# Kernel optimization log

Hardware: AMD Instinct MI355X
Metric: run time of the kernel (lower is better)

Reference implementation:

```python
import jax, jax.numpy as jnp
import numpy as np

MEMORY_SIZE = 32768
FEATURE_DIM = 128
BATCH = 4096


def setup_inputs() -> dict:
    key = jax.random.key(0)
    k1, k2, k3, k4 = jax.random.split(key, 4)
    memory = jax.random.normal(k1, (MEMORY_SIZE, FEATURE_DIM), dtype=jnp.float32)
    input_data = jax.random.normal(k2, (BATCH, FEATURE_DIM), dtype=jnp.float32)
    write_weights = jax.random.uniform(k3, (BATCH, MEMORY_SIZE), dtype=jnp.float32)
    query = jax.random.normal(k4, (BATCH, FEATURE_DIM), dtype=jnp.float32)
    return {"memory": memory, "input_data": input_data,
            "write_weights": write_weights, "query": query}


def reference(memory, input_data, write_weights, query):
    # ---- write(): row-normalize weights, scatter-accumulate into memory ----
    # The original python double-loop computes update[j] += w[i,j] * x[i],
    # i.e. update = w_norm.T @ x  -- a single GEMM.
    w_norm = write_weights / jnp.sum(write_weights, axis=1, keepdims=True)
    update = jnp.einsum('bm,bf->mf', w_norm, input_data)  # [M, F]
    memory_new = memory + update

    # ---- read(): softmax attention over memory slots ----
    scores = jnp.matmul(query, memory_new.T)              # [B, M]
    attention_weights = jax.nn.softmax(scores, axis=1)
    retrieved_memory = jnp.matmul(attention_weights, memory_new)  # [B, F]
    confidence_scores = jnp.max(attention_weights, axis=1)        # [B]
    return retrieved_memory, confidence_scores, memory_new
```

## Files before the change

kernel.cpp:

```cpp
#include <hip/hip_runtime.h>
#include <hip/hip_bf16.h>
#include <math.h>

#define MEMSZ 32768
#define FDIM  128
#define BATCH 4096

typedef float f32x4 __attribute__((ext_vector_type(4)));
typedef _Float16 f16x8 __attribute__((ext_vector_type(8)));
typedef short bf16x8 __attribute__((ext_vector_type(8)));
typedef unsigned short u16t;
typedef unsigned int u32t;

static __device__ __forceinline__ u16t f2h_bits(float f) {
    union { _Float16 h; u16t u; } c;
    c.h = (_Float16)f;
    return c.u;
}

#define GLDS16(gsrc, ldst) \
  __builtin_amdgcn_global_load_lds((const __attribute__((address_space(1))) void*)(gsrc), \
                                   (__attribute__((address_space(3))) void*)(ldst), 16, 0, 0)

__global__ __launch_bounds__(256) void k_rowsum(const float* __restrict__ W,
                                                float* __restrict__ inv_s) {
    const int row = blockIdx.x;
    const float4* Wr = reinterpret_cast<const float4*>(W + (size_t)row * MEMSZ);
    float acc = 0.f;
    #pragma unroll 4
    for (int i = threadIdx.x; i < MEMSZ / 4; i += 256) {
        float4 v = Wr[i];
        acc += (v.x + v.y) + (v.z + v.w);
    }
    #pragma unroll
    for (int off = 32; off > 0; off >>= 1)
        acc += __shfl_down(acc, off, 64);
    __shared__ float wsum[4];
    const int lane = threadIdx.x & 63, wid = threadIdx.x >> 6;
    if (lane == 0) wsum[wid] = acc;
    __syncthreads();
    if (threadIdx.x == 0)
        inv_s[row] = 1.0f / (wsum[0] + wsum[1] + wsum[2] + wsum[3]);
}

__global__ __launch_bounds__(256) void k_prep(const float* __restrict__ X,
                                              const float* __restrict__ inv_s,
                                              unsigned char* __restrict__ XT64) {
    __shared__ float xs[64][132];
    const int T = blockIdx.x;
    const int b0 = T * 64;
    const int tid = threadIdx.x;
    #pragma unroll
    for (int i = 0; i < 8; ++i) {
        const int idx = tid + i * 256;
        const int row = idx >> 5, c4 = idx & 31;
        const float s = inv_s[b0 + row];
        float4 v = *reinterpret_cast<const float4*>(&X[(size_t)(b0 + row) * FDIM + c4 * 4]);
        v.x *= s; v.y *= s; v.z *= s; v.w *= s;
        *reinterpret_cast<float4*>(&xs[row][c4 * 4]) = v;
    }
    __syncthreads();
    #pragma unroll
    for (int i = 0; i < 4; ++i) {
        const int L = tid + i * 256;
        const int fh = L >> 9, ff = (L >> 7) & 3, ks = (L >> 6) & 1, ln = L & 63;
        const int f = fh * 64 + ff * 16 + (ln & 15);
        const int bi = ks * 32 + (ln >> 4) * 8;
        u32t pk[4];
        #pragma unroll
        for (int h = 0; h < 4; ++h) {
            const float lo = xs[bi + 2 * h][f];
            const float hi = xs[bi + 2 * h + 1][f];
            asm("v_cvt_pk_bf16_f32 %0, %1, %2" : "=v"(pk[h]) : "v"(lo), "v"(hi));
        }
        *reinterpret_cast<uint4*>(XT64 + (size_t)T * 16384 + (size_t)L * 16) =
            make_uint4(pk[0], pk[1], pk[2], pk[3]);
    }
}

#define K2B 64
#define K2M 64
__global__ __launch_bounds__(256, 4) void k_update_sk(
    const float* __restrict__ W, const unsigned char* __restrict__ XT64,
    float* __restrict__ P)
{
    __shared__ __align__(16) unsigned char wt[2][16384];

    const int tid = threadIdx.x;
    const int lane = tid & 63, w = tid >> 6;
    const int q16 = lane & 15, g = lane >> 4;
    const int wm = w >> 1, wf = w & 1;
    const int mblk = (blockIdx.x >> 1) * K2M;
    const int khalf = blockIdx.x & 1;
    const int base = khalf * 32;

    f32x4 acc[2][4];
    #pragma unroll
    for (int mf = 0; mf < 2; ++mf)
        #pragma unroll
        for (int ff = 0; ff < 4; ++ff) acc[mf][ff] = (f32x4){0.f, 0.f, 0.f, 0.f};

    const unsigned char* xbase = XT64 + (size_t)(wf * 8192 + lane * 16);

    auto stageW = [&](int buf, int t) {
        const int b0 = t * K2B;
        #pragma unroll
        for (int c = 0; c < 4; ++c) {
            const int gi = c * 256 + tid;
            const int b = gi >> 4;
            const int src = ((gi & 15) * 16) ^ ((b & 8) << 1);
            GLDS16((const unsigned char*)W + (size_t)(b0 + b) * (MEMSZ * 4) + (size_t)mblk * 4 + src,
                   &wt[buf][gi * 16]);
        }
    };
    auto loadB = [&](bf16x8 (&br)[4][2], int t) {
        const unsigned char* xp = xbase + (size_t)t * 16384;
        #pragma unroll
        for (int ff = 0; ff < 4; ++ff)
            #pragma unroll
            for (int ks = 0; ks < 2; ++ks)
                br[ff][ks] = *reinterpret_cast<const bf16x8*>(xp + ff * 2048 + ks * 1024);
    };
    auto compute = [&](int buf, bf16x8 (&br)[4][2]) {
        bf16x8 afr[2][2];
        const unsigned char* tb = &wt[buf][0];
        #pragma unroll
        for (int mf = 0; mf < 2; ++mf) {
            const int mm4 = (wm * 32 + mf * 16 + q16) * 4;
            #pragma unroll
            for (int ks = 0; ks < 2; ++ks) {
                float av[8];
                #pragma unroll
                for (int e = 0; e < 8; ++e) {
                    const int b = ks * 32 + g * 8 + e;
                    av[e] = *reinterpret_cast<const float*>(
                        tb + b * 256 + (mm4 ^ ((b & 8) << 1)));
                }
                union { u32t u[4]; bf16x8 v; } cv;
                #pragma unroll
                for (int h = 0; h < 4; ++h)
                    asm("v_cvt_pk_bf16_f32 %0, %1, %2" : "=v"(cv.u[h]) : "v"(av[2 * h]), "v"(av[2 * h + 1]));
                afr[mf][ks] = cv.v;
            }
        }
        #pragma unroll
        for (int mf = 0; mf < 2; ++mf)
            #pragma unroll
            for (int ff = 0; ff < 4; ++ff)
                #pragma unroll
                for (int ks = 0; ks < 2; ++ks)
                    acc[mf][ff] = __builtin_amdgcn_mfma_f32_16x16x32_bf16(
                        afr[mf][ks], br[ff][ks], acc[mf][ff], 0, 0, 0);
    };

    bf16x8 bA[4][2], bB_[4][2];
    stageW(0, base); loadB(bA, base);
    const int NT = 32;
    for (int t = 0; t < NT; t += 2) {
        __builtin_amdgcn_s_barrier();
        if (t + 1 < NT) {
            loadB(bB_, base + t + 1); stageW(1, base + t + 1);
            asm volatile("s_waitcnt vmcnt(12)" ::: "memory");
        } else asm volatile("s_waitcnt vmcnt(0)" ::: "memory");
        __builtin_amdgcn_s_barrier();
        __builtin_amdgcn_sched_barrier(0);
        compute(0, bA);
        __builtin_amdgcn_s_barrier();
        if (t + 2 < NT) {
            loadB(bA, base + t + 2); stageW(0, base + t + 2);
            asm volatile("s_waitcnt vmcnt(12)" ::: "memory");
        } else asm volatile("s_waitcnt vmcnt(0)" ::: "memory");
        __builtin_amdgcn_s_barrier();
        __builtin_amdgcn_sched_barrier(0);
        compute(1, bB_);
    }

    float* Pk = P + (size_t)khalf * MEMSZ * FDIM;
    #pragma unroll
    for (int mf = 0; mf < 2; ++mf) {
        #pragma unroll
        for (int ff = 0; ff < 4; ++ff) {
            const int m0 = mblk + wm * 32 + mf * 16 + g * 4;
            const int fcol = wf * 64 + ff * 16 + q16;
            #pragma unroll
            for (int r = 0; r < 4; ++r)
                Pk[(size_t)(m0 + r) * FDIM + fcol] = acc[mf][ff][r];
        }
    }
}

__global__ __launch_bounds__(256) void k_fin(const float* __restrict__ Mem,
                                             const float* __restrict__ P,
                                             float* __restrict__ MemNew,
                                             u16t* __restrict__ MemH,
                                             u16t* __restrict__ MemHT) {
    const int tid = threadIdx.x;
    const int lane = tid & 63, w = tid >> 6;
    const int q16 = lane & 15, g = lane >> 4;
    const int wm = w >> 1, wf = w & 1;
    const int mblk = blockIdx.x * 64;
    const float* P0 = P;
    const float* P1 = P + (size_t)MEMSZ * FDIM;
    #pragma unroll
    for (int mf = 0; mf < 2; ++mf) {
        #pragma unroll
        for (int ff = 0; ff < 4; ++ff) {
            const int m0 = mblk + wm * 32 + mf * 16 + g * 4;
            const int fcol = wf * 64 + ff * 16 + q16;
            ushort4 ht;
            u16t* htp = reinterpret_cast<u16t*>(&ht);
            #pragma unroll
            for (int r = 0; r < 4; ++r) {
                const size_t idx = (size_t)(m0 + r) * FDIM + fcol;
                const float v = Mem[idx] + P0[idx] + P1[idx];
                MemNew[idx] = v;
                const u16t hb = f2h_bits(v);
                MemH[idx] = hb;
                htp[r] = hb;
            }
            *reinterpret_cast<ushort4*>(&MemHT[(size_t)fcol * MEMSZ + m0]) = ht;
        }
    }
}

__global__ __launch_bounds__(256, 2) void k_update_mfma(
    const float* __restrict__ W, const unsigned char* __restrict__ XT64,
    const float* __restrict__ Mem, float* __restrict__ MemNew,
    u16t* __restrict__ MemH, u16t* __restrict__ MemHT)
{
    __shared__ __align__(16) unsigned char wt[2][16384];

    const int tid = threadIdx.x;
    const int lane = tid & 63, w = tid >> 6;
    const int q16 = lane & 15, g = lane >> 4;
    const int wm = w >> 1, wf = w & 1;
    const int mblk = blockIdx.x * K2M;

    f32x4 acc[2][4];
    #pragma unroll
    for (int mf = 0; mf < 2; ++mf)
        #pragma unroll
        for (int ff = 0; ff < 4; ++ff) acc[mf][ff] = (f32x4){0.f, 0.f, 0.f, 0.f};

    const unsigned char* xbase = XT64 + (size_t)(wf * 8192 + lane * 16);

    auto stageW = [&](int buf, int t) {
        const int b0 = t * K2B;
        #pragma unroll
        for (int c = 0; c < 4; ++c) {
            const int gi = c * 256 + tid;
            const int b = gi >> 4;
            const int src = ((gi & 15) * 16) ^ ((b & 8) << 1);
            GLDS16((const unsigned char*)W + (size_t)(b0 + b) * (MEMSZ * 4) + (size_t)mblk * 4 + src,
                   &wt[buf][gi * 16]);
        }
    };
    auto loadB = [&](bf16x8 (&br)[4][2], int t) {
        const unsigned char* xp = xbase + (size_t)t * 16384;
        #pragma unroll
        for (int ff = 0; ff < 4; ++ff)
            #pragma unroll
            for (int ks = 0; ks < 2; ++ks)
                br[ff][ks] = *reinterpret_cast<const bf16x8*>(xp + ff * 2048 + ks * 1024);
    };
    auto compute = [&](int buf, bf16x8 (&br)[4][2]) {
        bf16x8 afr[2][2];
        const unsigned char* tb = &wt[buf][0];
        #pragma unroll
        for (int mf = 0; mf < 2; ++mf) {
            const int mm4 = (wm * 32 + mf * 16 + q16) * 4;
            #pragma unroll
            for (int ks = 0; ks < 2; ++ks) {
                float av[8];
                #pragma unroll
                for (int e = 0; e < 8; ++e) {
                    const int b = ks * 32 + g * 8 + e;
                    av[e] = *reinterpret_cast<const float*>(
                        tb + b * 256 + (mm4 ^ ((b & 8) << 1)));
                }
                union { u32t u[4]; bf16x8 v; } cv;
                #pragma unroll
                for (int h = 0; h < 4; ++h)
                    asm("v_cvt_pk_bf16_f32 %0, %1, %2" : "=v"(cv.u[h]) : "v"(av[2 * h]), "v"(av[2 * h + 1]));
                afr[mf][ks] = cv.v;
            }
        }
        #pragma unroll
        for (int mf = 0; mf < 2; ++mf)
            #pragma unroll
            for (int ff = 0; ff < 4; ++ff)
                #pragma unroll
                for (int ks = 0; ks < 2; ++ks)
                    acc[mf][ff] = __builtin_amdgcn_mfma_f32_16x16x32_bf16(
                        afr[mf][ks], br[ff][ks], acc[mf][ff], 0, 0, 0);
    };

    bf16x8 bA[4][2], bB_[4][2];
    stageW(0, 0); loadB(bA, 0);
    const int NT = BATCH / K2B;
    for (int t = 0; t < NT; t += 2) {
        __builtin_amdgcn_s_barrier();
        if (t + 1 < NT) { loadB(bB_, t + 1); stageW(1, t + 1); }
        if (t + 1 < NT) asm volatile("s_waitcnt vmcnt(12)" ::: "memory");
        else            asm volatile("s_waitcnt vmcnt(0)"  ::: "memory");
        __builtin_amdgcn_s_barrier();
        __builtin_amdgcn_sched_barrier(0);
        compute(0, bA);
        __builtin_amdgcn_s_barrier();
        if (t + 2 < NT) { loadB(bA, t + 2); stageW(0, t + 2); }
        if (t + 2 < NT) asm volatile("s_waitcnt vmcnt(12)" ::: "memory");
        else            asm volatile("s_waitcnt vmcnt(0)"  ::: "memory");
        __builtin_amdgcn_s_barrier();
        __builtin_amdgcn_sched_barrier(0);
        compute(1, bB_);
    }

    #pragma unroll
    for (int mf = 0; mf < 2; ++mf) {
        #pragma unroll
        for (int ff = 0; ff < 4; ++ff) {
            const int m0 = mblk + wm * 32 + mf * 16 + g * 4;
            const int fcol = wf * 64 + ff * 16 + q16;
            ushort4 ht;
            u16t* htp = reinterpret_cast<u16t*>(&ht);
            #pragma unroll
            for (int r = 0; r < 4; ++r) {
                const size_t idx = (size_t)(m0 + r) * FDIM + fcol;
                const float v = acc[mf][ff][r] + Mem[idx];
                MemNew[idx] = v;
                const u16t hb = f2h_bits(v);
                MemH[idx] = hb;
                htp[r] = hb;
            }
            *reinterpret_cast<ushort4*>(&MemHT[(size_t)fcol * MEMSZ + m0]) = ht;
        }
    }
}

#define K2_IT 16
#define K2_MT 64
__global__ __launch_bounds__(256) void k_update_f32(const float* __restrict__ W,
                                                    const float* __restrict__ X,
                                                    const float* __restrict__ inv_s,
                                                    const float* __restrict__ Mem,
                                                    float* __restrict__ MemNew) {
    __shared__ float w_lds[2][K2_IT][K2_MT];
    __shared__ float x_lds[2][K2_IT][FDIM];
    const int j0 = blockIdx.x * K2_MT;
    const int tid = threadIdx.x;
    const int tf = tid & 15;
    const int tj = tid >> 4;

    float acc[4][8];
    #pragma unroll
    for (int a = 0; a < 4; ++a)
        #pragma unroll
        for (int b = 0; b < 8; ++b) acc[a][b] = 0.f;

    float4 pw, px0, px1;
    float ps0, ps1;
    const int wr = tid >> 4, wc4 = tid & 15;
    const int xr0 = tid >> 5, xc0 = tid & 31;
    const int xr1 = (tid + 256) >> 5, xc1 = tid & 31;

    auto load_tile = [&](int it) {
        const int i0 = it * K2_IT;
        pw  = *reinterpret_cast<const float4*>(&W[(size_t)(i0 + wr) * MEMSZ + j0 + wc4 * 4]);
        px0 = *reinterpret_cast<const float4*>(&X[(size_t)(i0 + xr0) * FDIM + xc0 * 4]);
        ps0 = inv_s[i0 + xr0];
        px1 = *reinterpret_cast<const float4*>(&X[(size_t)(i0 + xr1) * FDIM + xc1 * 4]);
        ps1 = inv_s[i0 + xr1];
    };
    auto write_tile = [&](int buf) {
        *reinterpret_cast<float4*>(&w_lds[buf][wr][wc4 * 4]) = pw;
        float4 v = px0; v.x *= ps0; v.y *= ps0; v.z *= ps0; v.w *= ps0;
        *reinterpret_cast<float4*>(&x_lds[buf][xr0][xc0 * 4]) = v;
        float4 u = px1; u.x *= ps1; u.y *= ps1; u.z *= ps1; u.w *= ps1;
        *reinterpret_cast<float4*>(&x_lds[buf][xr1][xc1 * 4]) = u;
    };

    load_tile(0);
    write_tile(0);
    __syncthreads();
    const int NT = BATCH / K2_IT;
    for (int it = 0; it < NT; ++it) {
        const int cur = it & 1;
        if (it + 1 < NT) load_tile(it + 1);
        #pragma unroll 4
        for (int i = 0; i < K2_IT; ++i) {
            const float4 wv = *reinterpret_cast<const float4*>(&w_lds[cur][i][tj * 4]);
            const float4 xa = *reinterpret_cast<const float4*>(&x_lds[cur][i][tf * 4]);
            const float4 xb = *reinterpret_cast<const float4*>(&x_lds[cur][i][tf * 4 + 64]);
            const float wj[4] = {wv.x, wv.y, wv.z, wv.w};
            #pragma unroll
            for (int a = 0; a < 4; ++a) {
                acc[a][0] += wj[a] * xa.x; acc[a][1] += wj[a] * xa.y;
                acc[a][2] += wj[a] * xa.z; acc[a][3] += wj[a] * xa.w;
                acc[a][4] += wj[a] * xb.x; acc[a][5] += wj[a] * xb.y;
                acc[a][6] += wj[a] * xb.z; acc[a][7] += wj[a] * xb.w;
            }
        }
        if (it + 1 < NT) write_tile(cur ^ 1);
        __syncthreads();
    }
    #pragma unroll
    for (int a = 0; a < 4; ++a) {
        const size_t j = (size_t)j0 + tj * 4 + a;
        const float4 m0 = *reinterpret_cast<const float4*>(&Mem[j * FDIM + tf * 4]);
        const float4 m1 = *reinterpret_cast<const float4*>(&Mem[j * FDIM + tf * 4 + 64]);
        float4 o0 = {acc[a][0] + m0.x, acc[a][1] + m0.y, acc[a][2] + m0.z, acc[a][3] + m0.w};
        float4 o1 = {acc[a][4] + m1.x, acc[a][5] + m1.y, acc[a][6] + m1.z, acc[a][7] + m1.w};
        *reinterpret_cast<float4*>(&MemNew[j * FDIM + tf * 4]) = o0;
        *reinterpret_cast<float4*>(&MemNew[j * FDIM + tf * 4 + 64]) = o1;
    }
}

__global__ __launch_bounds__(256) void k_attn_mfma(
    const float* __restrict__ Q, const u16t* __restrict__ Kh, const u16t* __restrict__ KhT,
    float* __restrict__ accP, float* __restrict__ mP, float* __restrict__ lP, int s_shift)
{
    __shared__ __align__(16) unsigned char kv_u8[2][16384];
    __shared__ __align__(16) unsigned char v_u8[2][16384];
    __shared__ __align__(16) unsigned char p_u8[4][2048];

    const int tid = threadIdx.x;
    const int w = tid >> 6, lane = tid & 63;
    const int q16 = lane & 15, g = lane >> 4;
    const int S = 1 << s_shift;
    const int s_idx = blockIdx.x & (S - 1);
    const int qb = blockIdx.x >> s_shift;
    const int chunk = MEMSZ >> s_shift;
    const int slot0 = s_idx * chunk;
    const int NT = chunk >> 6;

    f16x8 qfrag[2][4];
    #pragma unroll
    for (int qf = 0; qf < 2; ++qf) {
        const float* qrow = Q + (size_t)(qb * 128 + w * 32 + qf * 16 + q16) * FDIM;
        #pragma unroll
        for (int ks = 0; ks < 4; ++ks) {
            float tmp[8];
            *reinterpret_cast<float4*>(&tmp[0]) = *reinterpret_cast<const float4*>(&qrow[ks * 32 + g * 8]);
            *reinterpret_cast<float4*>(&tmp[4]) = *reinterpret_cast<const float4*>(&qrow[ks * 32 + g * 8 + 4]);
            f16x8 v;
            #pragma unroll
            for (int e = 0; e < 8; ++e) v[e] = (_Float16)tmp[e];
            qfrag[qf][ks] = v;
        }
    }

    auto stage = [&](int buf, int tile) {
        const unsigned char* kbase = (const unsigned char*)Kh + (size_t)(slot0 + tile * 64) * 256;
        const unsigned char* tbase = (const unsigned char*)KhT + (size_t)(slot0 + tile * 64) * 2;
        #pragma unroll
        for (int c = 0; c < 4; ++c) {
            const int C = w * 4 + c;
            const int pp = C * 1024 + lane * 16;
            {
                const int slot = pp >> 8;
                const int inner = (pp & 255) ^ ((slot & 7) << 4);
                GLDS16(kbase + slot * 256 + inner, &kv_u8[buf][C * 1024]);
            }
            {
                const int d = pp >> 7;
                const int inner = (pp & 127) ^ ((d & 7) << 4);
                GLDS16(tbase + (size_t)d * 65536 + inner, &v_u8[buf][C * 1024]);
            }
        }
    };

    float m_run[2] = {-3.0e38f, -3.0e38f};
    float l_run[2] = {0.f, 0.f};
    f32x4 acc_o[8][2];
    #pragma unroll
    for (int df = 0; df < 8; ++df)
        #pragma unroll
        for (int qf = 0; qf < 2; ++qf)
            acc_o[df][qf] = (f32x4){0.f, 0.f, 0.f, 0.f};

    stage(0, 0);
    asm volatile("s_waitcnt vmcnt(0)" ::: "memory");
    __builtin_amdgcn_s_barrier();
    __builtin_amdgcn_sched_barrier(0);

    int cur = 0;
    for (int t = 0; t < NT; ++t) {
        if (t + 1 < NT) stage(cur ^ 1, t + 1);

        f32x4 acc_s[4][2];
        #pragma unroll
        for (int sf = 0; sf < 4; ++sf) {
            acc_s[sf][0] = (f32x4){0.f, 0.f, 0.f, 0.f};
            acc_s[sf][1] = (f32x4){0.f, 0.f, 0.f, 0.f};
        }
        const unsigned char* kvb = &kv_u8[cur][0];
        #pragma unroll
        for (int ks = 0; ks < 4; ++ks) {
            #pragma unroll
            for (int sf = 0; sf < 4; ++sf) {
                const int slot = sf * 16 + q16;
                const f16x8 a = *reinterpret_cast<const f16x8*>(
                    kvb + slot * 256 + ((ks * 64 + g * 16) ^ ((slot & 7) << 4)));
                acc_s[sf][0] = __builtin_amdgcn_mfma_f32_16x16x32_f16(a, qfrag[0][ks], acc_s[sf][0], 0, 0, 0);
                acc_s[sf][1] = __builtin_amdgcn_mfma_f32_16x16x32_f16(a, qfrag[1][ks], acc_s[sf][1], 0, 0, 0);
            }
        }

        f16x8 pb[2][2];
        unsigned char* pw = &p_u8[w][0];
        #pragma unroll
        for (int qf = 0; qf < 2; ++qf) {
            float pmax = acc_s[0][qf][0];
            #pragma unroll
            for (int sf = 0; sf < 4; ++sf)
                #pragma unroll
                for (int r = 0; r < 4; ++r)
                    pmax = fmaxf(pmax, acc_s[sf][qf][r]);
            pmax = fmaxf(pmax, __shfl_xor(pmax, 16));
            pmax = fmaxf(pmax, __shfl_xor(pmax, 32));
            const float mn = fmaxf(m_run[qf], pmax);
            float p[4][4];
            float psum = 0.f;
            #pragma unroll
            for (int sf = 0; sf < 4; ++sf)
                #pragma unroll
                for (int r = 0; r < 4; ++r) {
                    p[sf][r] = __expf(acc_s[sf][qf][r] - mn);
                    psum += p[sf][r];
                }
            psum += __shfl_xor(psum, 16);
            psum += __shfl_xor(psum, 32);
            const float sc = __expf(m_run[qf] - mn);
            l_run[qf] = l_run[qf] * sc + psum;
            m_run[qf] = mn;
            #pragma unroll
            for (int df = 0; df < 8; ++df) {
                acc_o[df][qf][0] *= sc; acc_o[df][qf][1] *= sc;
                acc_o[df][qf][2] *= sc; acc_o[df][qf][3] *= sc;
            }
            #pragma unroll
            for (int sf = 0; sf < 4; ++sf)
                #pragma unroll
                for (int rr = 0; rr < 2; ++rr) {
                    const u32t val = (u32t)f2h_bits(p[sf][2 * rr]) | ((u32t)f2h_bits(p[sf][2 * rr + 1]) << 16);
                    const int byte = q16 * 128 + (((sf * 16 + g * 4 + 2 * rr) * 2) ^ ((q16 & 7) << 4));
                    *reinterpret_cast<u32t*>(pw + byte) = val;
                }
            #pragma unroll
            for (int kk = 0; kk < 2; ++kk) {
                const int byte = q16 * 128 + (((kk * 32 + g * 8) * 2) ^ ((q16 & 7) << 4));
                pb[qf][kk] = *reinterpret_cast<const f16x8*>(pw + byte);
            }
        }

        const unsigned char* vb = &v_u8[cur][0];
        #pragma unroll
        for (int df = 0; df < 8; ++df) {
            #pragma unroll
            for (int kk = 0; kk < 2; ++kk) {
                const int d = df * 16 + q16;
                const f16x8 av = *reinterpret_cast<const f16x8*>(
                    vb + d * 128 + ((kk * 64 + g * 16) ^ ((d & 7) << 4)));
                acc_o[df][0] = __builtin_amdgcn_mfma_f32_16x16x32_f16(av, pb[0][kk], acc_o[df][0], 0, 0, 0);
                acc_o[df][1] = __builtin_amdgcn_mfma_f32_16x16x32_f16(av, pb[1][kk], acc_o[df][1], 0, 0, 0);
            }
        }

        asm volatile("s_waitcnt vmcnt(0)" ::: "memory");
        __builtin_amdgcn_s_barrier();
        __builtin_amdgcn_sched_barrier(0);
        cur ^= 1;
    }

    const int rowbase = qb * 128 + w * 32;
    #pragma unroll
    for (int qf = 0; qf < 2; ++qf) {
        const int row = rowbase + qf * 16 + q16;
        float* ap = accP + ((size_t)s_idx * BATCH + row) * FDIM;
        #pragma unroll
        for (int df = 0; df < 8; ++df) {
            float4 o = {acc_o[df][qf][0], acc_o[df][qf][1], acc_o[df][qf][2], acc_o[df][qf][3]};
            *reinterpret_cast<float4*>(&ap[df * 16 + g * 4]) = o;
        }
        if (g == 0) {
            mP[(size_t)s_idx * BATCH + row] = m_run[qf];
            lP[(size_t)s_idx * BATCH + row] = l_run[qf];
        }
    }
}

__global__ __launch_bounds__(256) void k_combine(const float* __restrict__ mP,
                                                 const float* __restrict__ lP,
                                                 const float* __restrict__ accP,
                                                 float* __restrict__ Out,
                                                 float* __restrict__ Conf, int S) {
    const int row = blockIdx.x * 8 + (threadIdx.x >> 5);
    const int lane = threadIdx.x & 31;
    float mt = -3.0e38f;
    for (int s = 0; s < S; ++s) mt = fmaxf(mt, mP[(size_t)s * BATCH + row]);
    float lt = 0.f;
    for (int s = 0; s < S; ++s) lt += lP[(size_t)s * BATCH + row] * __expf(mP[(size_t)s * BATCH + row] - mt);
    const float inv = 1.0f / lt;
    float4 o = {0.f, 0.f, 0.f, 0.f};
    for (int s = 0; s < S; ++s) {
        const float wgt = __expf(mP[(size_t)s * BATCH + row] - mt);
        const float4 a = *reinterpret_cast<const float4*>(&accP[((size_t)s * BATCH + row) * FDIM + lane * 4]);
        o.x += wgt * a.x; o.y += wgt * a.y; o.z += wgt * a.z; o.w += wgt * a.w;
    }
    float4 res = {o.x * inv, o.y * inv, o.z * inv, o.w * inv};
    *reinterpret_cast<float4*>(&Out[(size_t)row * FDIM + lane * 4]) = res;
    if (lane == 0) Conf[row] = inv;
}

#define QT 16
#define MT 64
#define LSTR (FDIM + 4)
__global__ __launch_bounds__(256) void k_attn_f32(const float* __restrict__ Q,
                                                  const float* __restrict__ MemNew,
                                                  float* __restrict__ Out,
                                                  float* __restrict__ Conf) {
    __shared__ float mem_lds[MT][LSTR];
    __shared__ float q_lds[QT][LSTR];
    __shared__ float p_lds[QT][MT];
    __shared__ float m_lds[QT], l_lds[QT], scale_lds[QT];

    const int tid = threadIdx.x;
    const int qblk = blockIdx.x * QT;

    #pragma unroll
    for (int r = 0; r < 2; ++r) {
        const int idx = tid + r * 256;
        const int row = idx >> 5, c4 = idx & 31;
        *reinterpret_cast<float4*>(&q_lds[row][c4 * 4]) =
            *reinterpret_cast<const float4*>(&Q[(size_t)(qblk + row) * FDIM + c4 * 4]);
    }
    if (tid < QT) { m_lds[tid] = -3.0e38f; l_lds[tid] = 0.f; }

    const int sq = (tid >> 5) * 2;
    const int sm = tid & 31;
    const int pq = tid >> 4;
    const int pf = (tid & 15) * 4;

    float acc[8];
    #pragma unroll
    for (int e = 0; e < 8; ++e) acc[e] = 0.f;

    for (int mt = 0; mt < MEMSZ / MT; ++mt) {
        __syncthreads();
        const float* src = MemNew + (size_t)mt * MT * FDIM;
        #pragma unroll
        for (int r = 0; r < 8; ++r) {
            const int idx = tid + r * 256;
            const int row = idx >> 5, c4 = idx & 31;
            *reinterpret_cast<float4*>(&mem_lds[row][c4 * 4]) =
                *reinterpret_cast<const float4*>(&src[(size_t)row * FDIM + c4 * 4]);
        }
        const float mold0 = m_lds[sq], mold1 = m_lds[sq + 1];
        __syncthreads();

        float s00 = 0.f, s01 = 0.f, s10 = 0.f, s11 = 0.f;
        #pragma unroll 8
        for (int k = 0; k < FDIM; k += 4) {
            const float4 qa = *reinterpret_cast<const float4*>(&q_lds[sq][k]);
            const float4 qb = *reinterpret_cast<const float4*>(&q_lds[sq + 1][k]);
            const float4 ma = *reinterpret_cast<const float4*>(&mem_lds[sm][k]);
            const float4 mb = *reinterpret_cast<const float4*>(&mem_lds[sm + 32][k]);
            s00 += qa.x*ma.x + qa.y*ma.y + qa.z*ma.z + qa.w*ma.w;
            s01 += qa.x*mb.x + qa.y*mb.y + qa.z*mb.z + qa.w*mb.w;
            s10 += qb.x*ma.x + qb.y*ma.y + qb.z*ma.z + qb.w*ma.w;
            s11 += qb.x*mb.x + qb.y*mb.y + qb.z*mb.z + qb.w*mb.w;
        }
        float r0 = fmaxf(s00, s01), r1 = fmaxf(s10, s11);
        #pragma unroll
        for (int off = 1; off <= 16; off <<= 1) {
            r0 = fmaxf(r0, __shfl_xor(r0, off, 64));
            r1 = fmaxf(r1, __shfl_xor(r1, off, 64));
        }
        const float mn0 = fmaxf(mold0, r0), mn1 = fmaxf(mold1, r1);
        const float p00 = __expf(s00 - mn0), p01 = __expf(s01 - mn0);
        const float p10 = __expf(s10 - mn1), p11 = __expf(s11 - mn1);
        float t0 = p00 + p01, t1 = p10 + p11;
        #pragma unroll
        for (int off = 1; off <= 16; off <<= 1) {
            t0 += __shfl_xor(t0, off, 64);
            t1 += __shfl_xor(t1, off, 64);
        }
        p_lds[sq][sm]      = p00; p_lds[sq][sm + 32]     = p01;
        p_lds[sq + 1][sm]  = p10; p_lds[sq + 1][sm + 32] = p11;
        if (sm == 0) {
            const float sc0 = __expf(mold0 - mn0), sc1 = __expf(mold1 - mn1);
            m_lds[sq] = mn0; m_lds[sq + 1] = mn1;
            l_lds[sq]     = l_lds[sq]     * sc0 + t0;
            l_lds[sq + 1] = l_lds[sq + 1] * sc1 + t1;
            scale_lds[sq] = sc0; scale_lds[sq + 1] = sc1;
        }
        __syncthreads();

        const float sc = scale_lds[pq];
        #pragma unroll
        for (int e = 0; e < 8; ++e) acc[e] *= sc;
        #pragma unroll 8
        for (int m = 0; m < MT; ++m) {
            const float p = p_lds[pq][m];
            const float4 va = *reinterpret_cast<const float4*>(&mem_lds[m][pf]);
            const float4 vb = *reinterpret_cast<const float4*>(&mem_lds[m][pf + 64]);
            acc[0] += p * va.x; acc[1] += p * va.y; acc[2] += p * va.z; acc[3] += p * va.w;
            acc[4] += p * vb.x; acc[5] += p * vb.y; acc[6] += p * vb.z; acc[7] += p * vb.w;
        }
    }
    const float linv = 1.0f / l_lds[pq];
    float4 o0 = {acc[0]*linv, acc[1]*linv, acc[2]*linv, acc[3]*linv};
    float4 o1 = {acc[4]*linv, acc[5]*linv, acc[6]*linv, acc[7]*linv};
    *reinterpret_cast<float4*>(&Out[(size_t)(qblk + pq) * FDIM + pf]) = o0;
    *reinterpret_cast<float4*>(&Out[(size_t)(qblk + pq) * FDIM + pf + 64]) = o1;
    if (tid < QT) Conf[qblk + tid] = 1.0f / l_lds[tid];
}

extern "C" void kernel_launch(void* const* d_in, const int* in_sizes, int n_in,
                              void* d_out, int out_size, void* d_ws, size_t ws_size,
                              hipStream_t stream) {
    (void)in_sizes; (void)n_in; (void)out_size;
    const float* memory   = (const float*)d_in[0];
    const float* input    = (const float*)d_in[1];
    const float* wweights = (const float*)d_in[2];
    const float* query    = (const float*)d_in[3];

    float* out       = (float*)d_out;
    float* retrieved = out;
    float* conf      = out + (size_t)BATCH * FDIM;
    float* mem_new   = conf + BATCH;

    char* ws = (char*)d_ws;
    float* inv_s = (float*)ws;
    const size_t off_xt   = 16384;
    const size_t off_h    = off_xt + (size_t)FDIM * BATCH * 2;
    const size_t off_hT   = off_h + (size_t)MEMSZ * FDIM * 2;
    const size_t off_part = off_hT + (size_t)MEMSZ * FDIM * 2;
    const size_t sz_p16   = (size_t)16 * ((size_t)BATCH * 8 + (size_t)BATCH * FDIM * 4);
    const size_t off_pk   = off_part + sz_p16;
    const size_t need_full = off_pk + (size_t)2 * MEMSZ * FDIM * 4;

    k_rowsum<<<BATCH, 256, 0, stream>>>(wweights, inv_s);

    if (ws_size >= need_full) {
        unsigned char* xt64 = (unsigned char*)(ws + off_xt);
        u16t* mh  = (u16t*)(ws + off_h);
        u16t* mhT = (u16t*)(ws + off_hT);
        float* mP   = (float*)(ws + off_part);
        float* lP   = mP + (size_t)16 * BATCH;
        float* accP = lP + (size_t)16 * BATCH;
        float* pk   = (float*)(ws + off_pk);
        k_prep<<<BATCH / 64, 256, 0, stream>>>(input, inv_s, xt64);
        k_update_sk<<<(MEMSZ / K2M) * 2, 256, 0, stream>>>(wweights, xt64, pk);
        k_fin<<<MEMSZ / 64, 256, 0, stream>>>(memory, pk, mem_new, mh, mhT);
        k_attn_mfma<<<(BATCH / 128) * 16, 256, 0, stream>>>(query, mh, mhT, accP, mP, lP, 4);
        k_combine<<<BATCH / 8, 256, 0, stream>>>(mP, lP, accP, retrieved, conf, 16);
        return;
    }

    int s_shift = -1;
    for (int sh = 4; sh >= 0; --sh) {
        const size_t S = (size_t)1 << sh;
        const size_t need = off_part + S * ((size_t)BATCH * 8 + (size_t)BATCH * FDIM * 4);
        if (ws_size >= need) { s_shift = sh; break; }
    }
    if (s_shift >= 0) {
        const int S = 1 << s_shift;
        unsigned char* xt64 = (unsigned char*)(ws + off_xt);
        u16t* mh  = (u16t*)(ws + off_h);
        u16t* mhT = (u16t*)(ws + off_hT);
        float* mP   = (float*)(ws + off_part);
        float* lP   = mP + (size_t)S * BATCH;
        float* accP = lP + (size_t)S * BATCH;
        k_prep<<<BATCH / 64, 256, 0, stream>>>(input, inv_s, xt64);
        k_update_mfma<<<MEMSZ / K2M, 256, 0, stream>>>(wweights, xt64, memory, mem_new, mh, mhT);
        k_attn_mfma<<<(BATCH / 128) * S, 256, 0, stream>>>(query, mh, mhT, accP, mP, lP, s_shift);
        k_combine<<<BATCH / 8, 256, 0, stream>>>(mP, lP, accP, retrieved, conf, S);
    } else {
        k_update_f32<<<MEMSZ / K2_MT, 256, 0, stream>>>(wweights, input, inv_s, memory, mem_new);
        k_attn_f32<<<BATCH / QT, 256, 0, stream>>>(query, mem_new, retrieved, conf);
    }
}
```

Measured before the change: 455.0 us.

## Fuse rowsum with bf16 transpose of write weights; drop split-K update

The row-sum kernel now also writes a transposed bf16 copy of the write weights, emitting per-tile partial sums that a small kernel reduces into inverse row sums. The update GEMM then streams this half-size, pre-transposed bf16 matrix over the full batch without split-K. That removes the fp32 partial buffers and the separate finalize kernel, since memory is added in the epilogue. The attention kernel also raises wave priority around its MFMA loops. The cost is an extra 256 MB bf16 write and read of the weights, and fewer blocks in the update kernel, which lowers its parallelism.

```diff
diff --git a/kernel.cpp b/kernel.cpp
--- a/kernel.cpp
+++ b/kernel.cpp
@@ -22,25 +22,72 @@
   __builtin_amdgcn_global_load_lds((const __attribute__((address_space(1))) void*)(gsrc), \
                                    (__attribute__((address_space(3))) void*)(ldst), 16, 0, 0)
 
-__global__ __launch_bounds__(256) void k_rowsum(const float* __restrict__ W,
-                                                float* __restrict__ inv_s) {
-    const int row = blockIdx.x;
-    const float4* Wr = reinterpret_cast<const float4*>(W + (size_t)row * MEMSZ);
-    float acc = 0.f;
-    #pragma unroll 4
-    for (int i = threadIdx.x; i < MEMSZ / 4; i += 256) {
-        float4 v = Wr[i];
-        acc += (v.x + v.y) + (v.z + v.w);
-    }
-    #pragma unroll
-    for (int off = 32; off > 0; off >>= 1)
-        acc += __shfl_down(acc, off, 64);
-    __shared__ float wsum[4];
-    const int lane = threadIdx.x & 63, wid = threadIdx.x >> 6;
-    if (lane == 0) wsum[wid] = acc;
+__global__ __launch_bounds__(256, 2) void k_rowsumT(const float* __restrict__ W,
+                                                    float* __restrict__ partial,
+                                                    u16t* __restrict__ WT) {
+    __shared__ __align__(16) unsigned char xs[65536];
+    __shared__ float red[128];
+    const int tid = threadIdx.x;
+    const int bt = blockIdx.x & 31, mt = blockIdx.x >> 5;
+    const int b0 = bt * 128, m0 = mt * 128;
+
+    #pragma unroll
+    for (int c = 0; c < 16; ++c) {
+        const int gi = c * 256 + tid;
+        const int b = gi >> 5;
+        const int inner = ((gi & 31) * 16) ^ ((b & 7) << 4);
+        GLDS16((const unsigned char*)W + ((size_t)(b0 + b) * MEMSZ + m0) * 4 + inner,
+               &xs[gi * 16]);
+    }
+    asm volatile("s_waitcnt vmcnt(0)" ::: "memory");
     __syncthreads();
-    if (threadIdx.x == 0)
-        inv_s[row] = 1.0f / (wsum[0] + wsum[1] + wsum[2] + wsum[3]);
+
+    {
+        const int b = tid >> 1, half = tid & 1;
+        float s = 0.f;
+        #pragma unroll
+        for (int i = 0; i < 16; ++i) {
+            const int off = b * 512 + ((half * 256 + i * 16) ^ ((b & 7) << 4));
+            const float4 v = *reinterpret_cast<const float4*>(&xs[off]);
+            s += (v.x + v.y) + (v.z + v.w);
+        }
+        s += __shfl_xor(s, 1, 64);
+        if (half == 0) red[b] = s;
+    }
+
+    {
+        const int m = tid & 127, bh = tid >> 7;
+        u16t* dstrow = WT + (size_t)(m0 + m) * BATCH + b0 + bh * 64;
+        #pragma unroll
+        for (int ch = 0; ch < 8; ++ch) {
+            u32t pk[4];
+            #pragma unroll
+            for (int h = 0; h < 4; ++h) {
+                const int b1 = bh * 64 + ch * 8 + 2 * h;
+                const float lo = *reinterpret_cast<const float*>(
+                    &xs[(size_t)b1 * 512 + ((m * 4) ^ ((b1 & 7) << 4))]);
+                const float hi = *reinterpret_cast<const float*>(
+                    &xs[(size_t)(b1 + 1) * 512 + ((m * 4) ^ (((b1 + 1) & 7) << 4))]);
+                asm("v_cvt_pk_bf16_f32 %0, %1, %2" : "=v"(pk[h]) : "v"(lo), "v"(hi));
+            }
+            *reinterpret_cast<uint4*>(dstrow + ch * 8) = make_uint4(pk[0], pk[1], pk[2], pk[3]);
+        }
+    }
+    __syncthreads();
+    if (tid < 128) partial[(size_t)mt * BATCH + b0 + tid] = red[tid];
+}
+
+__global__ __launch_bounds__(256) void k_inv(const float* __restrict__ partial,
+                                             float* __restrict__ inv_s) {
+    const int b = blockIdx.x * 256 + threadIdx.x;
+    float s0 = 0.f, s1 = 0.f, s2 = 0.f, s3 = 0.f;
+    for (int mt = 0; mt < 256; mt += 4) {
+        s0 += partial[(size_t)mt * BATCH + b];
+        s1 += partial[(size_t)(mt + 1) * BATCH + b];
+        s2 += partial[(size_t)(mt + 2) * BATCH + b];
+        s3 += partial[(size_t)(mt + 3) * BATCH + b];
+    }
+    inv_s[b] = 1.0f / ((s0 + s1) + (s2 + s3));
 }
 
 __global__ __launch_bounds__(256) void k_prep(const float* __restrict__ X,
@@ -80,19 +127,18 @@
 
 #define K2B 64
 #define K2M 64
-__global__ __launch_bounds__(256, 4) void k_update_sk(
-    const float* __restrict__ W, const unsigned char* __restrict__ XT64,
-    float* __restrict__ P)
+__global__ __launch_bounds__(256, 2) void k_update_wt(
+    const u16t* __restrict__ WT, const unsigned char* __restrict__ XT64,
+    const float* __restrict__ Mem, float* __restrict__ MemNew,
+    u16t* __restrict__ MemH, u16t* __restrict__ MemHT)
 {
-    __shared__ __align__(16) unsigned char wt[2][16384];
+    __shared__ __align__(16) unsigned char wt[2][8192];
 
     const int tid = threadIdx.x;
     const int lane = tid & 63, w = tid >> 6;
     const int q16 = lane & 15, g = lane >> 4;
     const int wm = w >> 1, wf = w & 1;
-    const int mblk = (blockIdx.x >> 1) * K2M;
-    const int khalf = blockIdx.x & 1;
-    const int base = khalf * 32;
+    const int mblk = blockIdx.x * K2M;
 
     f32x4 acc[2][4];
     #pragma unroll
@@ -103,13 +149,13 @@
     const unsigned char* xbase = XT64 + (size_t)(wf * 8192 + lane * 16);
 
     auto stageW = [&](int buf, int t) {
-        const int b0 = t * K2B;
-        #pragma unroll
-        for (int c = 0; c < 4; ++c) {
+        #pragma unroll
+        for (int c = 0; c < 2; ++c) {
             const int gi = c * 256 + tid;
-            const int b = gi >> 4;
-            const int src = ((gi & 15) * 16) ^ ((b & 8) << 1);
-            GLDS16((const unsigned char*)W + (size_t)(b0 + b) * (MEMSZ * 4) + (size_t)mblk * 4 + src,
+            const int m_loc = gi >> 3;
+            const int inner = ((gi & 7) * 16) ^ ((m_loc & 7) << 4);
+            GLDS16((const unsigned char*)WT + (size_t)(mblk + m_loc) * (BATCH * 2)
+                       + (size_t)t * 128 + inner,
                    &wt[buf][gi * 16]);
         }
     };
@@ -126,21 +172,11 @@
         const unsigned char* tb = &wt[buf][0];
         #pragma unroll
         for (int mf = 0; mf < 2; ++mf) {
-            const int mm4 = (wm * 32 + mf * 16 + q16) * 4;
+            const int m_loc = wm * 32 + mf * 16 + q16;
             #pragma unroll
             for (int ks = 0; ks < 2; ++ks) {
-                float av[8];
-                #pragma unroll
-                for (int e = 0; e < 8; ++e) {
-                    const int b = ks * 32 + g * 8 + e;
-                    av[e] = *reinterpret_cast<const float*>(
-                        tb + b * 256 + (mm4 ^ ((b & 8) << 1)));
-                }
-                union { u32t u[4]; bf16x8 v; } cv;
-                #pragma unroll
-                for (int h = 0; h < 4; ++h)
-                    asm("v_cvt_pk_bf16_f32 %0, %1, %2" : "=v"(cv.u[h]) : "v"(av[2 * h]), "v"(av[2 * h + 1]));
-                afr[mf][ks] = cv.v;
+                const int byte = m_loc * 128 + ((ks * 64 + g * 16) ^ ((m_loc & 7) << 4));
+                afr[mf][ks] = *reinterpret_cast<const bf16x8*>(tb + byte);
             }
         }
         #pragma unroll
@@ -154,53 +190,25 @@
     };
 
     bf16x8 bA[4][2], bB_[4][2];
-    stageW(0, base); loadB(bA, base);
-    const int NT = 32;
+    stageW(0, 0); loadB(bA, 0);
+    const int NT = BATCH / K2B;
     for (int t = 0; t < NT; t += 2) {
         __builtin_amdgcn_s_barrier();
-        if (t + 1 < NT) {
-            loadB(bB_, base + t + 1); stageW(1, base + t + 1);
-            asm volatile("s_waitcnt vmcnt(12)" ::: "memory");
-        } else asm volatile("s_waitcnt vmcnt(0)" ::: "memory");
+        if (t + 1 < NT) { loadB(bB_, t + 1); stageW(1, t + 1); }
+        if (t + 1 < NT) asm volatile("s_waitcnt vmcnt(10)" ::: "memory");
+        else            asm volatile("s_waitcnt vmcnt(0)"  ::: "memory");
         __builtin_amdgcn_s_barrier();
         __builtin_amdgcn_sched_barrier(0);
         compute(0, bA);
         __builtin_amdgcn_s_barrier();
-        if (t + 2 < NT) {
-            loadB(bA, base + t + 2); stageW(0, base + t + 2);
-            asm volatile("s_waitcnt vmcnt(12)" ::: "memory");
-        } else asm volatile("s_waitcnt vmcnt(0)" ::: "memory");
+        if (t + 2 < NT) { loadB(bA, t + 2); stageW(0, t + 2); }
+        if (t + 2 < NT) asm volatile("s_waitcnt vmcnt(10)" ::: "memory");
+        else            asm volatile("s_waitcnt vmcnt(0)"  ::: "memory");
         __builtin_amdgcn_s_barrier();
         __builtin_amdgcn_sched_barrier(0);
         compute(1, bB_);
     }
 
-    float* Pk = P + (size_t)khalf * MEMSZ * FDIM;
-    #pragma unroll
-    for (int mf = 0; mf < 2; ++mf) {
-        #pragma unroll
-        for (int ff = 0; ff < 4; ++ff) {
-            const int m0 = mblk + wm * 32 + mf * 16 + g * 4;
-            const int fcol = wf * 64 + ff * 16 + q16;
-            #pragma unroll
-            for (int r = 0; r < 4; ++r)
-                Pk[(size_t)(m0 + r) * FDIM + fcol] = acc[mf][ff][r];
-        }
-    }
-}
-
-__global__ __launch_bounds__(256) void k_fin(const float* __restrict__ Mem,
-                                             const float* __restrict__ P,
-                                             float* __restrict__ MemNew,
-                                             u16t* __restrict__ MemH,
-                                             u16t* __restrict__ MemHT) {
-    const int tid = threadIdx.x;
-    const int lane = tid & 63, w = tid >> 6;
-    const int q16 = lane & 15, g = lane >> 4;
-    const int wm = w >> 1, wf = w & 1;
-    const int mblk = blockIdx.x * 64;
-    const float* P0 = P;
-    const float* P1 = P + (size_t)MEMSZ * FDIM;
     #pragma unroll
     for (int mf = 0; mf < 2; ++mf) {
         #pragma unroll
@@ -212,7 +220,7 @@
             #pragma unroll
             for (int r = 0; r < 4; ++r) {
                 const size_t idx = (size_t)(m0 + r) * FDIM + fcol;
-                const float v = Mem[idx] + P0[idx] + P1[idx];
+                const float v = acc[mf][ff][r] + Mem[idx];
                 MemNew[idx] = v;
                 const u16t hb = f2h_bits(v);
                 MemH[idx] = hb;
@@ -337,84 +345,6 @@
     }
 }
 
-#define K2_IT 16
-#define K2_MT 64
-__global__ __launch_bounds__(256) void k_update_f32(const float* __restrict__ W,
-                                                    const float* __restrict__ X,
-                                                    const float* __restrict__ inv_s,
-                                                    const float* __restrict__ Mem,
-                                                    float* __restrict__ MemNew) {
-    __shared__ float w_lds[2][K2_IT][K2_MT];
-    __shared__ float x_lds[2][K2_IT][FDIM];
-    const int j0 = blockIdx.x * K2_MT;
-    const int tid = threadIdx.x;
-    const int tf = tid & 15;
-    const int tj = tid >> 4;
-
-    float acc[4][8];
-    #pragma unroll
-    for (int a = 0; a < 4; ++a)
-        #pragma unroll
-        for (int b = 0; b < 8; ++b) acc[a][b] = 0.f;
-
-    float4 pw, px0, px1;
-    float ps0, ps1;
-    const int wr = tid >> 4, wc4 = tid & 15;
-    const int xr0 = tid >> 5, xc0 = tid & 31;
-    const int xr1 = (tid + 256) >> 5, xc1 = tid & 31;
-
-    auto load_tile = [&](int it) {
-        const int i0 = it * K2_IT;
-        pw  = *reinterpret_cast<const float4*>(&W[(size_t)(i0 + wr) * MEMSZ + j0 + wc4 * 4]);
-        px0 = *reinterpret_cast<const float4*>(&X[(size_t)(i0 + xr0) * FDIM + xc0 * 4]);
-        ps0 = inv_s[i0 + xr0];
-        px1 = *reinterpret_cast<const float4*>(&X[(size_t)(i0 + xr1) * FDIM + xc1 * 4]);
-        ps1 = inv_s[i0 + xr1];
-    };
-    auto write_tile = [&](int buf) {
-        *reinterpret_cast<float4*>(&w_lds[buf][wr][wc4 * 4]) = pw;
-        float4 v = px0; v.x *= ps0; v.y *= ps0; v.z *= ps0; v.w *= ps0;
-        *reinterpret_cast<float4*>(&x_lds[buf][xr0][xc0 * 4]) = v;
-        float4 u = px1; u.x *= ps1; u.y *= ps1; u.z *= ps1; u.w *= ps1;
-        *reinterpret_cast<float4*>(&x_lds[buf][xr1][xc1 * 4]) = u;
-    };
-
-    load_tile(0);
-    write_tile(0);
-    __syncthreads();
-    const int NT = BATCH / K2_IT;
-    for (int it = 0; it < NT; ++it) {
-        const int cur = it & 1;
-        if (it + 1 < NT) load_tile(it + 1);
-        #pragma unroll 4
-        for (int i = 0; i < K2_IT; ++i) {
-            const float4 wv = *reinterpret_cast<const float4*>(&w_lds[cur][i][tj * 4]);
-            const float4 xa = *reinterpret_cast<const float4*>(&x_lds[cur][i][tf * 4]);
-            const float4 xb = *reinterpret_cast<const float4*>(&x_lds[cur][i][tf * 4 + 64]);
-            const float wj[4] = {wv.x, wv.y, wv.z, wv.w};
-            #pragma unroll
-            for (int a = 0; a < 4; ++a) {
-                acc[a][0] += wj[a] * xa.x; acc[a][1] += wj[a] * xa.y;
-                acc[a][2] += wj[a] * xa.z; acc[a][3] += wj[a] * xa.w;
-                acc[a][4] += wj[a] * xb.x; acc[a][5] += wj[a] * xb.y;
-                acc[a][6] += wj[a] * xb.z; acc[a][7] += wj[a] * xb.w;
-            }
-        }
-        if (it + 1 < NT) write_tile(cur ^ 1);
-        __syncthreads();
-    }
-    #pragma unroll
-    for (int a = 0; a < 4; ++a) {
-        const size_t j = (size_t)j0 + tj * 4 + a;
-        const float4 m0 = *reinterpret_cast<const float4*>(&Mem[j * FDIM + tf * 4]);
-        const float4 m1 = *reinterpret_cast<const float4*>(&Mem[j * FDIM + tf * 4 + 64]);
-        float4 o0 = {acc[a][0] + m0.x, acc[a][1] + m0.y, acc[a][2] + m0.z, acc[a][3] + m0.w};
-        float4 o1 = {acc[a][4] + m1.x, acc[a][5] + m1.y, acc[a][6] + m1.z, acc[a][7] + m1.w};
-        *reinterpret_cast<float4*>(&MemNew[j * FDIM + tf * 4]) = o0;
-        *reinterpret_cast<float4*>(&MemNew[j * FDIM + tf * 4 + 64]) = o1;
-    }
-}
-
 __global__ __launch_bounds__(256) void k_attn_mfma(
     const float* __restrict__ Q, const u16t* __restrict__ Kh, const u16t* __restrict__ KhT,
     float* __restrict__ accP, float* __restrict__ mP, float* __restrict__ lP, int s_shift)
@@ -494,6 +424,7 @@
             acc_s[sf][1] = (f32x4){0.f, 0.f, 0.f, 0.f};
         }
         const unsigned char* kvb = &kv_u8[cur][0];
+        __builtin_amdgcn_s_setprio(1);
         #pragma unroll
         for (int ks = 0; ks < 4; ++ks) {
             #pragma unroll
@@ -505,6 +436,7 @@
                 acc_s[sf][1] = __builtin_amdgcn_mfma_f32_16x16x32_f16(a, qfrag[1][ks], acc_s[sf][1], 0, 0, 0);
             }
         }
+        __builtin_amdgcn_s_setprio(0);
 
         f16x8 pb[2][2];
         unsigned char* pw = &p_u8[w][0];
@@ -554,6 +486,7 @@
         }
 
         const unsigned char* vb = &v_u8[cur][0];
+        __builtin_amdgcn_s_setprio(1);
         #pragma unroll
         for (int df = 0; df < 8; ++df) {
             #pragma unroll
@@ -565,6 +498,7 @@
                 acc_o[df][1] = __builtin_amdgcn_mfma_f32_16x16x32_f16(av, pb[1][kk], acc_o[df][1], 0, 0, 0);
             }
         }
+        __builtin_amdgcn_s_setprio(0);
 
         asm volatile("s_waitcnt vmcnt(0)" ::: "memory");
         __builtin_amdgcn_s_barrier();
@@ -612,6 +546,105 @@
     if (lane == 0) Conf[row] = inv;
 }
 
+__global__ __launch_bounds__(256) void k_rowsum(const float* __restrict__ W,
+                                                float* __restrict__ inv_s) {
+    const int row = blockIdx.x;
+    const float4* Wr = reinterpret_cast<const float4*>(W + (size_t)row * MEMSZ);
+    float acc = 0.f;
+    #pragma unroll 4
+    for (int i = threadIdx.x; i < MEMSZ / 4; i += 256) {
+        float4 v = Wr[i];
+        acc += (v.x + v.y) + (v.z + v.w);
+    }
+    #pragma unroll
+    for (int off = 32; off > 0; off >>= 1)
+        acc += __shfl_down(acc, off, 64);
+    __shared__ float wsum[4];
+    const int lane = threadIdx.x & 63, wid = threadIdx.x >> 6;
+    if (lane == 0) wsum[wid] = acc;
+    __syncthreads();
+    if (threadIdx.x == 0)
+        inv_s[row] = 1.0f / (wsum[0] + wsum[1] + wsum[2] + wsum[3]);
+}
+
+#define K2_IT 16
+#define K2_MT 64
+__global__ __launch_bounds__(256) void k_update_f32(const float* __restrict__ W,
+                                                    const float* __restrict__ X,
+                                                    const float* __restrict__ inv_s,
+                                                    const float* __restrict__ Mem,
+                                                    float* __restrict__ MemNew) {
+    __shared__ float w_lds[2][K2_IT][K2_MT];
+    __shared__ float x_lds[2][K2_IT][FDIM];
+    const int j0 = blockIdx.x * K2_MT;
+    const int tid = threadIdx.x;
+    const int tf = tid & 15;
+    const int tj = tid >> 4;
+
+    float acc[4][8];
+    #pragma unroll
+    for (int a = 0; a < 4; ++a)
+        #pragma unroll
+        for (int b = 0; b < 8; ++b) acc[a][b] = 0.f;
+
+    float4 pw, px0, px1;
+    float ps0, ps1;
+    const int wr = tid >> 4, wc4 = tid & 15;
+    const int xr0 = tid >> 5, xc0 = tid & 31;
+    const int xr1 = (tid + 256) >> 5, xc1 = tid & 31;
+
+    auto load_tile = [&](int it) {
+        const int i0 = it * K2_IT;
+        pw  = *reinterpret_cast<const float4*>(&W[(size_t)(i0 + wr) * MEMSZ + j0 + wc4 * 4]);
+        px0 = *reinterpret_cast<const float4*>(&X[(size_t)(i0 + xr0) * FDIM + xc0 * 4]);
+        ps0 = inv_s[i0 + xr0];
+        px1 = *reinterpret_cast<const float4*>(&X[(size_t)(i0 + xr1) * FDIM + xc1 * 4]);
+        ps1 = inv_s[i0 + xr1];
+    };
+    auto write_tile = [&](int buf) {
+        *reinterpret_cast<float4*>(&w_lds[buf][wr][wc4 * 4]) = pw;
+        float4 v = px0; v.x *= ps0; v.y *= ps0; v.z *= ps0; v.w *= ps0;
+        *reinterpret_cast<float4*>(&x_lds[buf][xr0][xc0 * 4]) = v;
+        float4 u = px1; u.x *= ps1; u.y *= ps1; u.z *= ps1; u.w *= ps1;
+        *reinterpret_cast<float4*>(&x_lds[buf][xr1][xc1 * 4]) = u;
+    };
+
+    load_tile(0);
+    write_tile(0);
+    __syncthreads();
+    const int NT = BATCH / K2_IT;
+    for (int it = 0; it < NT; ++it) {
+        const int cur = it & 1;
+        if (it + 1 < NT) load_tile(it + 1);
+        #pragma unroll 4
+        for (int i = 0; i < K2_IT; ++i) {
+            const float4 wv = *reinterpret_cast<const float4*>(&w_lds[cur][i][tj * 4]);
+            const float4 xa = *reinterpret_cast<const float4*>(&x_lds[cur][i][tf * 4]);
+            const float4 xb = *reinterpret_cast<const float4*>(&x_lds[cur][i][tf * 4 + 64]);
+            const float wj[4] = {wv.x, wv.y, wv.z, wv.w};
+            #pragma unroll
+            for (int a = 0; a < 4; ++a) {
+                acc[a][0] += wj[a] * xa.x; acc[a][1] += wj[a] * xa.y;
+                acc[a][2] += wj[a] * xa.z; acc[a][3] += wj[a] * xa.w;
+                acc[a][4] += wj[a] * xb.x; acc[a][5] += wj[a] * xb.y;
+                acc[a][6] += wj[a] * xb.z; acc[a][7] += wj[a] * xb.w;
+            }
+        }
+        if (it + 1 < NT) write_tile(cur ^ 1);
+        __syncthreads();
+    }
+    #pragma unroll
+    for (int a = 0; a < 4; ++a) {
+        const size_t j = (size_t)j0 + tj * 4 + a;
+        const float4 m0 = *reinterpret_cast<const float4*>(&Mem[j * FDIM + tf * 4]);
+        const float4 m1 = *reinterpret_cast<const float4*>(&Mem[j * FDIM + tf * 4 + 64]);
+        float4 o0 = {acc[a][0] + m0.x, acc[a][1] + m0.y, acc[a][2] + m0.z, acc[a][3] + m0.w};
+        float4 o1 = {acc[a][4] + m1.x, acc[a][5] + m1.y, acc[a][6] + m1.z, acc[a][7] + m1.w};
+        *reinterpret_cast<float4*>(&MemNew[j * FDIM + tf * 4]) = o0;
+        *reinterpret_cast<float4*>(&MemNew[j * FDIM + tf * 4 + 64]) = o1;
+    }
+}
+
 #define QT 16
 #define MT 64
 #define LSTR (FDIM + 4)
@@ -737,10 +770,9 @@
     const size_t off_hT   = off_h + (size_t)MEMSZ * FDIM * 2;
     const size_t off_part = off_hT + (size_t)MEMSZ * FDIM * 2;
     const size_t sz_p16   = (size_t)16 * ((size_t)BATCH * 8 + (size_t)BATCH * FDIM * 4);
-    const size_t off_pk   = off_part + sz_p16;
-    const size_t need_full = off_pk + (size_t)2 * MEMSZ * FDIM * 4;
-
-    k_rowsum<<<BATCH, 256, 0, stream>>>(wweights, inv_s);
+    const size_t off_rp   = off_part + sz_p16;
+    const size_t off_wt   = off_rp + (size_t)256 * BATCH * 4;
+    const size_t need_full = off_wt + (size_t)MEMSZ * BATCH * 2;
 
     if (ws_size >= need_full) {
         unsigned char* xt64 = (unsigned char*)(ws + off_xt);
@@ -749,15 +781,19 @@
         float* mP   = (float*)(ws + off_part);
         float* lP   = mP + (size_t)16 * BATCH;
         float* accP = lP + (size_t)16 * BATCH;
-        float* pk   = (float*)(ws + off_pk);
+        float* rp   = (float*)(ws + off_rp);
+        u16t* wt    = (u16t*)(ws + off_wt);
+
+        k_rowsumT<<<32 * 256, 256, 0, stream>>>(wweights, rp, wt);
+        k_inv<<<BATCH / 256, 256, 0, stream>>>(rp, inv_s);
         k_prep<<<BATCH / 64, 256, 0, stream>>>(input, inv_s, xt64);
-        k_update_sk<<<(MEMSZ / K2M) * 2, 256, 0, stream>>>(wweights, xt64, pk);
-        k_fin<<<MEMSZ / 64, 256, 0, stream>>>(memory, pk, mem_new, mh, mhT);
+        k_update_wt<<<MEMSZ / K2M, 256, 0, stream>>>(wt, xt64, memory, mem_new, mh, mhT);
         k_attn_mfma<<<(BATCH / 128) * 16, 256, 0, stream>>>(query, mh, mhT, accP, mP, lP, 4);
         k_combine<<<BATCH / 8, 256, 0, stream>>>(mP, lP, accP, retrieved, conf, 16);
         return;
     }
 
+    k_rowsum<<<BATCH, 256, 0, stream>>>(wweights, inv_s);
     int s_shift = -1;
     for (int sh = 4; sh >= 0; --sh) {
         const size_t S = (size_t)1 << sh;
```

After: 468.2 us. 1.03x slower.
